# Optimization experiments

Hardware: AMD Instinct MI355X
Metric: run time of the kernel (lower is better)

Reference implementation:

```python
import jax, jax.numpy as jnp
import numpy as np

EPS = 1e-6  # flax LayerNorm default

def _layernorm(x, scale, bias):
    mu = jnp.mean(x, axis=-1, keepdims=True)
    var = jnp.mean(jnp.square(x - mu), axis=-1, keepdims=True)
    return (x - mu) * jax.lax.rsqrt(var + EPS) * scale + bias

def _rel_pos_index(ws):
    coords = np.stack(np.meshgrid(np.arange(ws), np.arange(ws), indexing='ij'))  # [2,ws,ws]
    cf = coords.reshape(2, -1)
    rel = (cf[:, :, None] - cf[:, None, :]).transpose(1, 2, 0)  # [N,N,2]
    rel[..., 0] += ws - 1
    rel[..., 1] += ws - 1
    rel[..., 0] *= 2 * ws - 1
    return rel.sum(-1)  # [N,N] in [0,(2ws-1)^2)

def setup_inputs() -> dict:
    key = jax.random.key(0)
    ks = jax.random.split(key, 8)
    B, H, W, C = 16, 56, 56, 384
    L, heads, ws = 2, 12, 7
    s = 0.02
    return {
        'x': jax.random.normal(ks[0], (B, H, W, C), jnp.float32),
        'ln1_s': jnp.ones((L, C), jnp.float32),
        'ln1_b': jnp.zeros((L, C), jnp.float32),
        'qkv_w': jax.random.normal(ks[1], (L, C, 3 * C), jnp.float32) * s,
        'rpb': jax.random.normal(ks[2], (L, (2 * ws - 1) ** 2, heads), jnp.float32) * s,
        'proj_w': jax.random.normal(ks[3], (L, C, C), jnp.float32) * s,
        'ln2_s': jnp.ones((L, C), jnp.float32),
        'ln2_b': jnp.zeros((L, C), jnp.float32),
        'mlp_w1': jax.random.normal(ks[4], (L, C, 4 * C), jnp.float32) * s,
        'mlp_b1': jnp.zeros((L, 4 * C), jnp.float32),
        'mlp_w2': jax.random.normal(ks[5], (L, 4 * C, C), jnp.float32) * s,
        'mlp_b2': jnp.zeros((L, C), jnp.float32),
        'window_size': 7,
    }

def reference(x, ln1_s, ln1_b, qkv_w, rpb, proj_w, ln2_s, ln2_b, mlp_w1, mlp_b1, mlp_w2, mlp_b2, window_size):
    B, H, W, C = x.shape
    ws = int(window_size)
    L = qkv_w.shape[0]
    heads = rpb.shape[-1]
    hd = C // heads
    N = ws * ws
    idx = jnp.asarray(_rel_pos_index(ws))  # [N,N] static

    # --- split to windows: [B,H,W,C] -> [B*nWh*nWw, N, C]
    xw = x.reshape(B, H // ws, ws, W // ws, ws, C)
    xw = xw.transpose(0, 1, 3, 2, 4, 5).reshape(-1, N, C)

    for l in range(L):
        # --- windowed MHSA with relative position bias
        h = _layernorm(xw, ln1_s[l], ln1_b[l])
        qkv = (h @ qkv_w[l]).reshape(-1, N, 3, heads, hd)
        q, k, v = qkv[:, :, 0], qkv[:, :, 1], qkv[:, :, 2]  # [nW,N,heads,hd]
        attn = jnp.einsum('wqhd,wkhd->whqk', q, k) * (hd ** -0.5)
        bias = rpb[l][idx].transpose(2, 0, 1)  # [heads,N,N]
        attn = jax.nn.softmax(attn + bias[None], axis=-1)
        o = jnp.einsum('whqk,wkhd->wqhd', attn, v).reshape(-1, N, C)
        xw = xw + o @ proj_w[l]
        # --- MLP block
        h = _layernorm(xw, ln2_s[l], ln2_b[l])
        h = jax.nn.gelu(h @ mlp_w1[l] + mlp_b1[l])
        xw = xw + (h @ mlp_w2[l] + mlp_b2[l])

    # --- merge windows back to [B,H,W,C]
    out = xw.reshape(B, H // ws, W // ws, ws, ws, C)
    out = out.transpose(0, 1, 3, 2, 4, 5).reshape(B, H, W, C)
    return out
```

## Files before the change

kernel.cpp:

```cpp
#include <hip/hip_runtime.h>
#include <hip/hip_bf16.h>

typedef __bf16 bf16;
typedef __attribute__((ext_vector_type(4))) __bf16 bf16x4;
typedef __attribute__((ext_vector_type(8))) __bf16 bf16x8;
typedef __attribute__((ext_vector_type(4))) float f32x4;

__device__ __forceinline__ void async_ld16(const void* g, void* l) {
    __builtin_amdgcn_global_load_lds(
        (const __attribute__((address_space(1))) unsigned int*)g,
        (__attribute__((address_space(3))) unsigned int*)l, 16, 0, 0);
}

__global__ __launch_bounds__(256) void k_f2bt(const float* __restrict__ in,
                                              bf16* __restrict__ out, int Kd, int Nd) {
    size_t loff = (size_t)blockIdx.y * Kd * Nd;
    int id = blockIdx.x * 256 + threadIdx.x;
    if (id >= Kd * Nd) return;
    int k = id / Nd, n = id - k * Nd;
    out[loff + (size_t)n * Kd + k] = (bf16)in[loff + id];
}

__global__ __launch_bounds__(256) void k_aux(const float* __restrict__ rpb,
                                             unsigned short* __restrict__ ridx,
                                             float* __restrict__ rpbT) {
    int e = blockIdx.x * 256 + threadIdx.x;
    if (e < 2401) {
        int i = e / 49, j = e - i * 49;
        int yi = i / 7, xi = i - yi * 7, yj = j / 7, xj = j - yj * 7;
        ridx[e] = (unsigned short)((yi - yj + 6) * 13 + (xi - xj + 6));
    }
    if (e < 4056) {
        int l = e / 2028, r = e - l * 2028;
        int h = r / 169, p = r - h * 169;
        rpbT[e] = rpb[l * 2028 + p * 12 + h];
    }
}

__global__ __launch_bounds__(256) void k_lnr(const float* __restrict__ x,
                                             const float* __restrict__ s,
                                             const float* __restrict__ b,
                                             float* __restrict__ xres,
                                             bf16* __restrict__ h) {
    int traw = blockIdx.x * 4 + (threadIdx.x >> 6);
    int lane = threadIdx.x & 63;
    int bb = traw / 3136;
    int rem = traw - bb * 3136;
    int y = rem / 56, xc = rem - y * 56;
    int w = bb * 64 + (y / 7) * 8 + (xc / 7);
    int n = (y % 7) * 7 + (xc % 7);
    int twin = w * 49 + n;

    const float4* row = (const float4*)(x + (size_t)traw * 384);
    float4 v0 = row[lane];
    float4 v1 = make_float4(0.f, 0.f, 0.f, 0.f);
    if (lane < 32) v1 = row[64 + lane];
    float sum = v0.x + v0.y + v0.z + v0.w + v1.x + v1.y + v1.z + v1.w;
#pragma unroll
    for (int m = 1; m < 64; m <<= 1) sum += __shfl_xor(sum, m);
    float mu = sum * (1.f / 384.f);
    float sq = (v0.x - mu) * (v0.x - mu) + (v0.y - mu) * (v0.y - mu) +
               (v0.z - mu) * (v0.z - mu) + (v0.w - mu) * (v0.w - mu);
    if (lane < 32)
        sq += (v1.x - mu) * (v1.x - mu) + (v1.y - mu) * (v1.y - mu) +
              (v1.z - mu) * (v1.z - mu) + (v1.w - mu) * (v1.w - mu);
#pragma unroll
    for (int m = 1; m < 64; m <<= 1) sq += __shfl_xor(sq, m);
    float r = rsqrtf(sq * (1.f / 384.f) + 1e-6f);

    float4* xr = (float4*)(xres + (size_t)twin * 384);
    const float4* s4 = (const float4*)s;
    const float4* b4 = (const float4*)b;
    bf16* ho = h + (size_t)twin * 384;
    {
        xr[lane] = v0;
        float4 sv = s4[lane], bv = b4[lane];
        bf16x4 ov;
        ov[0] = (bf16)((v0.x - mu) * r * sv.x + bv.x);
        ov[1] = (bf16)((v0.y - mu) * r * sv.y + bv.y);
        ov[2] = (bf16)((v0.z - mu) * r * sv.z + bv.z);
        ov[3] = (bf16)((v0.w - mu) * r * sv.w + bv.w);
        *(bf16x4*)&ho[lane * 4] = ov;
    }
    if (lane < 32) {
        xr[64 + lane] = v1;
        float4 sv = s4[64 + lane], bv = b4[64 + lane];
        bf16x4 ov;
        ov[0] = (bf16)((v1.x - mu) * r * sv.x + bv.x);
        ov[1] = (bf16)((v1.y - mu) * r * sv.y + bv.y);
        ov[2] = (bf16)((v1.z - mu) * r * sv.z + bv.z);
        ov[3] = (bf16)((v1.w - mu) * r * sv.w + bv.w);
        *(bf16x4*)&ho[256 + lane * 4] = ov;
    }
}

__global__ __launch_bounds__(256) void k_ln(const float* __restrict__ xres,
                                            const float* __restrict__ s,
                                            const float* __restrict__ b,
                                            bf16* __restrict__ h) {
    int t = blockIdx.x * 4 + (threadIdx.x >> 6);
    int lane = threadIdx.x & 63;
    const float4* row = (const float4*)(xres + (size_t)t * 384);
    float4 v0 = row[lane];
    float4 v1 = make_float4(0.f, 0.f, 0.f, 0.f);
    if (lane < 32) v1 = row[64 + lane];
    float sum = v0.x + v0.y + v0.z + v0.w + v1.x + v1.y + v1.z + v1.w;
#pragma unroll
    for (int m = 1; m < 64; m <<= 1) sum += __shfl_xor(sum, m);
    float mu = sum * (1.f / 384.f);
    float sq = (v0.x - mu) * (v0.x - mu) + (v0.y - mu) * (v0.y - mu) +
               (v0.z - mu) * (v0.z - mu) + (v0.w - mu) * (v0.w - mu);
    if (lane < 32)
        sq += (v1.x - mu) * (v1.x - mu) + (v1.y - mu) * (v1.y - mu) +
              (v1.z - mu) * (v1.z - mu) + (v1.w - mu) * (v1.w - mu);
#pragma unroll
    for (int m = 1; m < 64; m <<= 1) sq += __shfl_xor(sq, m);
    float r = rsqrtf(sq * (1.f / 384.f) + 1e-6f);
    const float4* s4 = (const float4*)s;
    const float4* b4 = (const float4*)b;
    bf16* ho = h + (size_t)t * 384;
    {
        float4 sv = s4[lane], bv = b4[lane];
        bf16x4 ov;
        ov[0] = (bf16)((v0.x - mu) * r * sv.x + bv.x);
        ov[1] = (bf16)((v0.y - mu) * r * sv.y + bv.y);
        ov[2] = (bf16)((v0.z - mu) * r * sv.z + bv.z);
        ov[3] = (bf16)((v0.w - mu) * r * sv.w + bv.w);
        *(bf16x4*)&ho[lane * 4] = ov;
    }
    if (lane < 32) {
        float4 sv = s4[64 + lane], bv = b4[64 + lane];
        bf16x4 ov;
        ov[0] = (bf16)((v1.x - mu) * r * sv.x + bv.x);
        ov[1] = (bf16)((v1.y - mu) * r * sv.y + bv.y);
        ov[2] = (bf16)((v1.z - mu) * r * sv.z + bv.z);
        ov[3] = (bf16)((v1.w - mu) * r * sv.w + bv.w);
        *(bf16x4*)&ho[256 + lane * 4] = ov;
    }
}

__device__ inline float gelu_f(float x) {
    float u = 0.7978845608028654f * (x + 0.044715f * x * x * x);
    float t = 1.f - 2.f / (__expf(2.f * u) + 1.f);
    return 0.5f * x * (1.f + t);
}

template <int EPI>
__global__ __launch_bounds__(256) void k_gemm(const bf16* __restrict__ A,
                                              const bf16* __restrict__ Bt,
                                              const float* __restrict__ bias,
                                              float* __restrict__ resid,
                                              bf16* __restrict__ Cout,
                                              float* __restrict__ outf,
                                              int N, int K) {
    __shared__ __align__(16) char lds[49152];
    int tid = threadIdx.x;

    int nwg = gridDim.x * gridDim.y;
    int orig = blockIdx.y * gridDim.x + blockIdx.x;
    int q = nwg >> 3, r8 = nwg & 7;
    int xcd = orig & 7, idx = orig >> 3;
    int wg = (xcd < r8 ? xcd * (q + 1) : r8 * (q + 1) + (xcd - r8) * q) + idx;
    int n0 = (wg % gridDim.x) * 128;
    int m0 = (wg / gridDim.x) * 128;

    int wave = tid >> 6, lane = tid & 63;
    int wm = (wave >> 1) * 64, wn = (wave & 1) * 64;
    int col = lane & 15, quad = lane >> 4;

    f32x4 acc[4][4] = {};

    int r0 = 2 * wave * 16 + (lane >> 2);
    int ksl = (lane & 3) ^ ((r0 >> 1) & 3);
    const bf16* ga0 = A + (size_t)(m0 + r0) * K + ksl * 8;
    const bf16* gb0 = Bt + (size_t)(n0 + r0) * K + ksl * 8;
    size_t rowK16 = (size_t)16 * K;
    int ldsoff = 2 * wave * 512;

    int NT = K >> 5;

    auto stage = [&](int t, int b) {
        const bf16* a = ga0 + t * 32;
        const bf16* g = gb0 + t * 32;
        char* base = (char*)lds + b * 16384;
        bf16* Ab = (bf16*)base;
        bf16* Bb = (bf16*)(base + 8192);
        async_ld16(a, Ab + ldsoff);
        async_ld16(a + rowK16, Ab + ldsoff + 512);
        async_ld16(g, Bb + ldsoff);
        async_ld16(g + rowK16, Bb + ldsoff + 512);
    };

    stage(0, 0);
    stage(1, 1);

    int buf = 0;
    for (int t = 0; t < NT; ++t) {
        if (t < NT - 1)
            asm volatile("s_waitcnt vmcnt(4) lgkmcnt(0)\n\ts_barrier" ::: "memory");
        else
            asm volatile("s_waitcnt vmcnt(0) lgkmcnt(0)\n\ts_barrier" ::: "memory");

        if (t + 2 < NT) {
            int sb = buf + 2; if (sb >= 3) sb -= 3;
            stage(t + 2, sb);
        }

        const char* base = (const char*)lds + buf * 16384;
        const bf16* Ab = (const bf16*)base;
        const bf16* Bb = (const bf16*)(base + 8192);
        bf16x8 af[4], bfv[4];
#pragma unroll
        for (int i = 0; i < 4; i++) {
            int ra = wm + i * 16 + col;
            af[i] = *(const bf16x8*)&Ab[ra * 32 + ((quad ^ ((ra >> 1) & 3)) << 3)];
            int rb = wn + i * 16 + col;
            bfv[i] = *(const bf16x8*)&Bb[rb * 32 + ((quad ^ ((rb >> 1) & 3)) << 3)];
        }
#pragma unroll
        for (int mi = 0; mi < 4; mi++)
#pragma unroll
            for (int ni = 0; ni < 4; ni++)
                acc[mi][ni] = __builtin_amdgcn_mfma_f32_16x16x32_bf16(
                    af[mi], bfv[ni], acc[mi][ni], 0, 0, 0);
        buf = (buf == 2) ? 0 : buf + 1;
    }

    __syncthreads();
    float* scrw = (float*)lds + wave * (16 * 68);

    int prow = lane >> 3;
    int pc0 = (lane & 7) * 8;
#pragma unroll
    for (int mi = 0; mi < 4; mi++) {
#pragma unroll
        for (int ni = 0; ni < 4; ni++)
#pragma unroll
            for (int r = 0; r < 4; r++)
                scrw[(quad * 4 + r) * 68 + ni * 16 + col] = acc[mi][ni][r];
#pragma unroll
        for (int h = 0; h < 2; h++) {
            int lr = h * 8 + prow;
            const float* sp = scrw + lr * 68 + pc0;
            float4 u0 = *(const float4*)sp;
            float4 u1 = *(const float4*)(sp + 4);
            int gm = m0 + wm + mi * 16 + lr;
            int gn = n0 + wn + pc0;
            size_t off = (size_t)gm * N + gn;
            if (EPI == 0) {
                bf16x8 ov;
                ov[0] = (bf16)u0.x; ov[1] = (bf16)u0.y; ov[2] = (bf16)u0.z; ov[3] = (bf16)u0.w;
                ov[4] = (bf16)u1.x; ov[5] = (bf16)u1.y; ov[6] = (bf16)u1.z; ov[7] = (bf16)u1.w;
                *(bf16x8*)&Cout[off] = ov;
            } else if (EPI == 1) {
                float4 b0 = *(const float4*)&bias[gn];
                float4 b1 = *(const float4*)&bias[gn + 4];
                bf16x8 ov;
                ov[0] = (bf16)gelu_f(u0.x + b0.x); ov[1] = (bf16)gelu_f(u0.y + b0.y);
                ov[2] = (bf16)gelu_f(u0.z + b0.z); ov[3] = (bf16)gelu_f(u0.w + b0.w);
                ov[4] = (bf16)gelu_f(u1.x + b1.x); ov[5] = (bf16)gelu_f(u1.y + b1.y);
                ov[6] = (bf16)gelu_f(u1.z + b1.z); ov[7] = (bf16)gelu_f(u1.w + b1.w);
                *(bf16x8*)&Cout[off] = ov;
            } else if (EPI == 2) {
                float4 r0v = *(const float4*)&resid[off];
                float4 r1v = *(const float4*)&resid[off + 4];
                r0v.x += u0.x; r0v.y += u0.y; r0v.z += u0.z; r0v.w += u0.w;
                r1v.x += u1.x; r1v.y += u1.y; r1v.z += u1.z; r1v.w += u1.w;
                *(float4*)&resid[off] = r0v;
                *(float4*)&resid[off + 4] = r1v;
            } else if (EPI == 3) {
                float4 b0 = *(const float4*)&bias[gn];
                float4 b1 = *(const float4*)&bias[gn + 4];
                float4 r0v = *(const float4*)&resid[off];
                float4 r1v = *(const float4*)&resid[off + 4];
                r0v.x += u0.x + b0.x; r0v.y += u0.y + b0.y;
                r0v.z += u0.z + b0.z; r0v.w += u0.w + b0.w;
                r1v.x += u1.x + b1.x; r1v.y += u1.y + b1.y;
                r1v.z += u1.z + b1.z; r1v.w += u1.w + b1.w;
                *(float4*)&resid[off] = r0v;
                *(float4*)&resid[off + 4] = r1v;
            } else {
                float4 b0 = *(const float4*)&bias[gn];
                float4 b1 = *(const float4*)&bias[gn + 4];
                float4 r0v = *(const float4*)&resid[off];
                float4 r1v = *(const float4*)&resid[off + 4];
                r0v.x += u0.x + b0.x; r0v.y += u0.y + b0.y;
                r0v.z += u0.z + b0.z; r0v.w += u0.w + b0.w;
                r1v.x += u1.x + b1.x; r1v.y += u1.y + b1.y;
                r1v.z += u1.z + b1.z; r1v.w += u1.w + b1.w;
                int wdx = gm / 49, n = gm - wdx * 49;
                int bb = wdx >> 6, r64 = wdx & 63;
                int n7 = n / 7;
                int yy = (r64 >> 3) * 7 + n7;
                int xx = (r64 & 7) * 7 + (n - n7 * 7);
                size_t traw = ((size_t)((bb * 56 + yy) * 56 + xx)) * 384 + gn;
                *(float4*)&outf[traw] = r0v;
                *(float4*)&outf[traw + 4] = r1v;
            }
        }
    }
}

__global__ __launch_bounds__(256) void k_attn(const bf16* __restrict__ qkv,
                                              const unsigned short* __restrict__ ridx,
                                              const float* __restrict__ rpbT,
                                              bf16* __restrict__ o) {
    __shared__ unsigned short relIdx[2401];
    __shared__ float rpbs[4][169];
    __shared__ __align__(16) bf16 Vs[4][32 * 72];
    __shared__ __align__(16) bf16 Ps[4][64 * 72];

    int tid = threadIdx.x;
    int wave = tid >> 6, lane = tid & 63;
    int col = lane & 15, quad = lane >> 4;
    int w = blockIdx.x;
    int head = blockIdx.y * 4 + wave;
    const float scale = 0.17677669529663687f;

    for (int e = tid; e < 2401; e += 256) relIdx[e] = ridx[e];
    for (int e = lane; e < 169; e += 64) rpbs[wave][e] = rpbT[head * 169 + e];

    const bf16* base = qkv + (size_t)w * 49 * 1152 + head * 32;
    bf16* vsw = Vs[wave];
    bf16* psw = Ps[wave];

    bf16x4 z4 = {(bf16)0.f, (bf16)0.f, (bf16)0.f, (bf16)0.f};
    for (int e = lane; e < 576; e += 64) *(bf16x4*)&vsw[e * 4] = z4;
    for (int e = lane; e < 392; e += 64) {
        int j = e >> 3, d4 = (e & 7) * 4;
        bf16x4 vv = *(const bf16x4*)&base[768 + (size_t)j * 1152 + d4];
        vsw[(d4 + 0) * 72 + j] = vv[0];
        vsw[(d4 + 1) * 72 + j] = vv[1];
        vsw[(d4 + 2) * 72 + j] = vv[2];
        vsw[(d4 + 3) * 72 + j] = vv[3];
    }

    __syncthreads();

    bf16x8 qf[4], kf[4];
#pragma unroll
    for (int mi = 0; mi < 4; mi++) {
        size_t row = (size_t)(mi * 16 + col) * 1152 + quad * 8;
        qf[mi] = *(const bf16x8*)&base[row];
        kf[mi] = *(const bf16x8*)&base[384 + row];
    }

    f32x4 S[4][4] = {};
#pragma unroll
    for (int mi = 0; mi < 4; mi++)
#pragma unroll
        for (int nj = 0; nj < 4; nj++)
            S[mi][nj] = __builtin_amdgcn_mfma_f32_16x16x32_bf16(qf[mi], kf[nj], S[mi][nj], 0, 0, 0);

    float* rp = rpbs[wave];
#pragma unroll
    for (int mi = 0; mi < 4; mi++) {
#pragma unroll
        for (int r = 0; r < 4; r++) {
            int ii = mi * 16 + quad * 4 + r;
            int ir = (ii < 49 ? ii : 0) * 49;
            float sv[4];
            float mx = -1e30f;
#pragma unroll
            for (int nj = 0; nj < 4; nj++) {
                int j = nj * 16 + col;
                float v;
                if (j < 49) v = S[mi][nj][r] * scale + rp[relIdx[ir + j]];
                else v = -1e30f;
                sv[nj] = v;
                mx = fmaxf(mx, v);
            }
#pragma unroll
            for (int m = 1; m < 16; m <<= 1) mx = fmaxf(mx, __shfl_xor(mx, m));
            float sum = 0.f;
#pragma unroll
            for (int nj = 0; nj < 4; nj++) {
                float p = __expf(sv[nj] - mx);
                sv[nj] = p;
                sum += p;
            }
#pragma unroll
            for (int m = 1; m < 16; m <<= 1) sum += __shfl_xor(sum, m);
            float is = 1.f / sum;
#pragma unroll
            for (int nj = 0; nj < 4; nj++)
                psw[ii * 72 + nj * 16 + col] = (bf16)(sv[nj] * is);
        }
    }

    __syncthreads();

    f32x4 O[4][2] = {};
#pragma unroll
    for (int kt = 0; kt < 2; kt++) {
        bf16x8 vb[2];
#pragma unroll
        for (int nt = 0; nt < 2; nt++)
            vb[nt] = *(const bf16x8*)&vsw[(nt * 16 + col) * 72 + kt * 32 + quad * 8];
#pragma unroll
        for (int mi = 0; mi < 4; mi++) {
            bf16x8 pa = *(const bf16x8*)&psw[(mi * 16 + col) * 72 + kt * 32 + quad * 8];
#pragma unroll
            for (int nt = 0; nt < 2; nt++)
                O[mi][nt] = __builtin_amdgcn_mfma_f32_16x16x32_bf16(pa, vb[nt], O[mi][nt], 0, 0, 0);
        }
    }

    bf16* ob = o + (size_t)w * 49 * 384 + head * 32;
#pragma unroll
    for (int mi = 0; mi < 4; mi++) {
#pragma unroll
        for (int r = 0; r < 4; r++) {
            int i = mi * 16 + quad * 4 + r;
            if (i < 49) {
#pragma unroll
                for (int nt = 0; nt < 2; nt++)
                    ob[(size_t)i * 384 + nt * 16 + col] = (bf16)O[mi][nt][r];
            }
        }
    }
}

extern "C" void kernel_launch(void* const* d_in, const int* in_sizes, int n_in,
                              void* d_out, int out_size, void* d_ws, size_t ws_size,
                              hipStream_t stream) {
    const float* x      = (const float*)d_in[0];
    const float* ln1_s  = (const float*)d_in[1];
    const float* ln1_b  = (const float*)d_in[2];
    const float* qkv_w  = (const float*)d_in[3];
    const float* rpb    = (const float*)d_in[4];
    const float* proj_w = (const float*)d_in[5];
    const float* ln2_s  = (const float*)d_in[6];
    const float* ln2_b  = (const float*)d_in[7];
    const float* mlp_w1 = (const float*)d_in[8];
    const float* mlp_b1 = (const float*)d_in[9];
    const float* mlp_w2 = (const float*)d_in[10];
    const float* mlp_b2 = (const float*)d_in[11];
    float* out = (float*)d_out;

    char* ws = (char*)d_ws;
    float* xres  = (float*)ws;
    bf16* qkvbuf = (bf16*)(ws + 77070336);
    bf16* obuf   = (bf16*)(ws + 192675840);
    bf16* wbuf   = (bf16*)(ws + 231211008);
    bf16* hidden = qkvbuf;
    bf16* hbuf   = (bf16*)d_out;

    unsigned short* ridx = (unsigned short*)((char*)d_out + 40000000);
    float* rpbT          = (float*)((char*)d_out + 40016384);

    bf16* qkvw_b  = wbuf;
    bf16* projw_b = wbuf + 884736;
    bf16* mlp1_b  = wbuf + 1179648;
    bf16* mlp2_b  = wbuf + 2359296;

    k_f2bt<<<dim3(1728, 2), 256, 0, stream>>>(qkv_w, qkvw_b, 384, 1152);
    k_f2bt<<<dim3(576, 2), 256, 0, stream>>>(proj_w, projw_b, 384, 384);
    k_f2bt<<<dim3(2304, 2), 256, 0, stream>>>(mlp_w1, mlp1_b, 384, 1536);
    k_f2bt<<<dim3(2304, 2), 256, 0, stream>>>(mlp_w2, mlp2_b, 1536, 384);
    k_aux<<<16, 256, 0, stream>>>(rpb, ridx, rpbT);

    k_lnr<<<12544, 256, 0, stream>>>(x, ln1_s, ln1_b, xres, hbuf);

    for (int l = 0; l < 2; l++) {
        k_gemm<0><<<dim3(9, 392), 256, 0, stream>>>(
            hbuf, qkvw_b + (size_t)l * 442368, nullptr, nullptr, qkvbuf, nullptr, 1152, 384);
        k_attn<<<dim3(1024, 3), 256, 0, stream>>>(qkvbuf, ridx, rpbT + l * 2028, obuf);
        k_gemm<2><<<dim3(3, 392), 256, 0, stream>>>(
            obuf, projw_b + (size_t)l * 147456, nullptr, xres, nullptr, nullptr, 384, 384);
        k_ln<<<12544, 256, 0, stream>>>(xres, ln2_s + l * 384, ln2_b + l * 384, hbuf);
        k_gemm<1><<<dim3(12, 392), 256, 0, stream>>>(
            hbuf, mlp1_b + (size_t)l * 589824, mlp_b1 + l * 1536, nullptr, hidden, nullptr, 1536, 384);
        if (l == 0) {
            k_gemm<3><<<dim3(3, 392), 256, 0, stream>>>(
                hidden, mlp2_b, mlp_b2, xres, nullptr, nullptr, 384, 1536);
            k_ln<<<12544, 256, 0, stream>>>(xres, ln1_s + 384, ln1_b + 384, hbuf);
        } else {
            k_gemm<4><<<dim3(3, 392), 256, 0, stream>>>(
                hidden, mlp2_b + 589824, mlp_b2 + 384, xres, nullptr, out, 384, 1536);
        }
    }
}
```

Baseline: 1.061 ms.

## Add 256x128-tile GEMM with triple-buffered LDS for QKV and MLP1

Adds a new GEMM kernel with a 256x128 output tile per workgroup (each wave computing 128x64), a three-stage async global-to-LDS pipeline, and an XCD-aware remapping of workgroup ids. It is used for the QKV projection and the first MLP layer, which halves the grid along M. The aim is more reuse of each loaded tile and better L2 locality per XCD. The cost is higher register pressure from 128 accumulator vectors per lane and 72KB of LDS per block, which limits occupancy.

New measurement: 1.091 ms. 1.03x slower.

```diff
diff --git a/kernel.cpp b/kernel.cpp
--- a/kernel.cpp
+++ b/kernel.cpp
@@ -301,6 +301,133 @@
     }
 }
 
+template <int EPI>
+__global__ __launch_bounds__(256, 2) void k_gemm_w(const bf16* __restrict__ A,
+                                                   const bf16* __restrict__ Bt,
+                                                   const float* __restrict__ bias,
+                                                   float* __restrict__ resid,
+                                                   bf16* __restrict__ Cout,
+                                                   float* __restrict__ outf,
+                                                   int N, int K) {
+    __shared__ __align__(16) char lds[73728];
+    int tid = threadIdx.x;
+
+    int nwg = gridDim.x * gridDim.y;
+    int orig = blockIdx.y * gridDim.x + blockIdx.x;
+    int q = nwg >> 3, r8 = nwg & 7;
+    int xcd = orig & 7, idx = orig >> 3;
+    int wg = (xcd < r8 ? xcd * (q + 1) : r8 * (q + 1) + (xcd - r8) * q) + idx;
+    int n0 = (wg % gridDim.x) * 128;
+    int m0 = (wg / gridDim.x) * 256;
+
+    int wave = tid >> 6, lane = tid & 63;
+    int wm = (wave >> 1) * 128, wn = (wave & 1) * 64;
+    int col = lane & 15, quad = lane >> 4;
+
+    f32x4 acc[8][4] = {};
+
+    int rr = lane >> 2;
+    int ksl = (lane & 3) ^ ((rr >> 1) & 3);
+    const bf16* ga0 = A + (size_t)(m0 + 64 * wave + rr) * K + ksl * 8;
+    const bf16* gb0 = Bt + (size_t)(n0 + 32 * wave + rr) * K + ksl * 8;
+    size_t rowK16 = (size_t)16 * K;
+    int ldsA = wave * 2048;
+    int ldsB = wave * 1024;
+
+    int NT = K >> 5;
+
+    auto stage = [&](int t, int b) {
+        const bf16* a = ga0 + t * 32;
+        const bf16* g = gb0 + t * 32;
+        char* base = (char*)lds + b * 24576;
+        bf16* Ab = (bf16*)base;
+        bf16* Bb = (bf16*)(base + 16384);
+        async_ld16(a, Ab + ldsA);
+        async_ld16(a + rowK16, Ab + ldsA + 512);
+        async_ld16(a + 2 * rowK16, Ab + ldsA + 1024);
+        async_ld16(a + 3 * rowK16, Ab + ldsA + 1536);
+        async_ld16(g, Bb + ldsB);
+        async_ld16(g + rowK16, Bb + ldsB + 512);
+    };
+
+    stage(0, 0);
+    stage(1, 1);
+
+    int buf = 0;
+    for (int t = 0; t < NT; ++t) {
+        if (t < NT - 1)
+            asm volatile("s_waitcnt vmcnt(6) lgkmcnt(0)\n\ts_barrier" ::: "memory");
+        else
+            asm volatile("s_waitcnt vmcnt(0) lgkmcnt(0)\n\ts_barrier" ::: "memory");
+
+        if (t + 2 < NT) {
+            int sb = buf + 2; if (sb >= 3) sb -= 3;
+            stage(t + 2, sb);
+        }
+
+        const char* base = (const char*)lds + buf * 24576;
+        const bf16* Ab = (const bf16*)base;
+        const bf16* Bb = (const bf16*)(base + 16384);
+        bf16x8 af[8], bfv[4];
+#pragma unroll
+        for (int i = 0; i < 8; i++) {
+            int ra = wm + i * 16 + col;
+            af[i] = *(const bf16x8*)&Ab[ra * 32 + ((quad ^ ((ra >> 1) & 3)) << 3)];
+        }
+#pragma unroll
+        for (int i = 0; i < 4; i++) {
+            int rb = wn + i * 16 + col;
+            bfv[i] = *(const bf16x8*)&Bb[rb * 32 + ((quad ^ ((rb >> 1) & 3)) << 3)];
+        }
+#pragma unroll
+        for (int mi = 0; mi < 8; mi++)
+#pragma unroll
+            for (int ni = 0; ni < 4; ni++)
+                acc[mi][ni] = __builtin_amdgcn_mfma_f32_16x16x32_bf16(
+                    af[mi], bfv[ni], acc[mi][ni], 0, 0, 0);
+        buf = (buf == 2) ? 0 : buf + 1;
+    }
+
+    __syncthreads();
+    float* scrw = (float*)lds + wave * (16 * 68);
+
+    int prow = lane >> 3;
+    int pc0 = (lane & 7) * 8;
+#pragma unroll
+    for (int mi = 0; mi < 8; mi++) {
+#pragma unroll
+        for (int ni = 0; ni < 4; ni++)
+#pragma unroll
+            for (int r = 0; r < 4; r++)
+                scrw[(quad * 4 + r) * 68 + ni * 16 + col] = acc[mi][ni][r];
+#pragma unroll
+        for (int h = 0; h < 2; h++) {
+            int lr = h * 8 + prow;
+            const float* sp = scrw + lr * 68 + pc0;
+            float4 u0 = *(const float4*)sp;
+            float4 u1 = *(const float4*)(sp + 4);
+            int gm = m0 + wm + mi * 16 + lr;
+            int gn = n0 + wn + pc0;
+            size_t off = (size_t)gm * N + gn;
+            if (EPI == 0) {
+                bf16x8 ov;
+                ov[0] = (bf16)u0.x; ov[1] = (bf16)u0.y; ov[2] = (bf16)u0.z; ov[3] = (bf16)u0.w;
+                ov[4] = (bf16)u1.x; ov[5] = (bf16)u1.y; ov[6] = (bf16)u1.z; ov[7] = (bf16)u1.w;
+                *(bf16x8*)&Cout[off] = ov;
+            } else {
+                float4 b0 = *(const float4*)&bias[gn];
+                float4 b1 = *(const float4*)&bias[gn + 4];
+                bf16x8 ov;
+                ov[0] = (bf16)gelu_f(u0.x + b0.x); ov[1] = (bf16)gelu_f(u0.y + b0.y);
+                ov[2] = (bf16)gelu_f(u0.z + b0.z); ov[3] = (bf16)gelu_f(u0.w + b0.w);
+                ov[4] = (bf16)gelu_f(u1.x + b1.x); ov[5] = (bf16)gelu_f(u1.y + b1.y);
+                ov[6] = (bf16)gelu_f(u1.z + b1.z); ov[7] = (bf16)gelu_f(u1.w + b1.w);
+                *(bf16x8*)&Cout[off] = ov;
+            }
+        }
+    }
+}
+
 __global__ __launch_bounds__(256) void k_attn(const bf16* __restrict__ qkv,
                                               const unsigned short* __restrict__ ridx,
                                               const float* __restrict__ rpbT,
@@ -463,13 +590,13 @@
     k_lnr<<<12544, 256, 0, stream>>>(x, ln1_s, ln1_b, xres, hbuf);
 
     for (int l = 0; l < 2; l++) {
-        k_gemm<0><<<dim3(9, 392), 256, 0, stream>>>(
+        k_gemm_w<0><<<dim3(9, 196), 256, 0, stream>>>(
             hbuf, qkvw_b + (size_t)l * 442368, nullptr, nullptr, qkvbuf, nullptr, 1152, 384);
         k_attn<<<dim3(1024, 3), 256, 0, stream>>>(qkvbuf, ridx, rpbT + l * 2028, obuf);
         k_gemm<2><<<dim3(3, 392), 256, 0, stream>>>(
             obuf, projw_b + (size_t)l * 147456, nullptr, xres, nullptr, nullptr, 384, 384);
         k_ln<<<12544, 256, 0, stream>>>(xres, ln2_s + l * 384, ln2_b + l * 384, hbuf);
-        k_gemm<1><<<dim3(12, 392), 256, 0, stream>>>(
+        k_gemm_w<1><<<dim3(12, 196), 256, 0, stream>>>(
             hbuf, mlp1_b + (size_t)l * 589824, mlp_b1 + l * 1536, nullptr, hidden, nullptr, 1536, 384);
         if (l == 0) {
             k_gemm<3><<<dim3(3, 392), 256, 0, stream>>>(
```

## Load GEMM B operand directly into registers and halve LDS footprint

Applied to the files above, without the earlier changes.

The GEMM no longer stages the weight (B) tile through LDS. Each wave now loads its B fragments straight from global memory into registers and prefetches the next k-step one iteration ahead. Only A stays triple-buffered in LDS, so shared memory drops to 24KB and launch bounds now request 4 blocks per CU, aiming for higher occupancy and less LDS traffic. In exchange, waves sharing the same columns fetch B redundantly from cache, and the extra in-flight register loads raise register pressure and vmcnt bookkeeping.

Measured after the change: 1.348 ms. +27.1%, slower.

```diff
diff --git a/kernel.cpp b/kernel.cpp
--- a/kernel.cpp
+++ b/kernel.cpp
@@ -146,14 +146,14 @@
 }
 
 template <int EPI>
-__global__ __launch_bounds__(256) void k_gemm(const bf16* __restrict__ A,
-                                              const bf16* __restrict__ Bt,
-                                              const float* __restrict__ bias,
-                                              float* __restrict__ resid,
-                                              bf16* __restrict__ Cout,
-                                              float* __restrict__ outf,
-                                              int N, int K) {
-    __shared__ __align__(16) char lds[49152];
+__global__ __launch_bounds__(256, 4) void k_gemm(const bf16* __restrict__ A,
+                                                 const bf16* __restrict__ Bt,
+                                                 const float* __restrict__ bias,
+                                                 float* __restrict__ resid,
+                                                 bf16* __restrict__ Cout,
+                                                 float* __restrict__ outf,
+                                                 int N, int K) {
+    __shared__ __align__(16) char lds[24576];
     int tid = threadIdx.x;
 
     int nwg = gridDim.x * gridDim.y;
@@ -173,61 +173,65 @@
     int r0 = 2 * wave * 16 + (lane >> 2);
     int ksl = (lane & 3) ^ ((r0 >> 1) & 3);
     const bf16* ga0 = A + (size_t)(m0 + r0) * K + ksl * 8;
-    const bf16* gb0 = Bt + (size_t)(n0 + r0) * K + ksl * 8;
     size_t rowK16 = (size_t)16 * K;
     int ldsoff = 2 * wave * 512;
 
+    const bf16* gB = Bt + (size_t)(n0 + wn + col) * K + quad * 8;
+    size_t fr16 = (size_t)16 * K;
+
     int NT = K >> 5;
 
-    auto stage = [&](int t, int b) {
+    auto stageA = [&](int t, int b) {
         const bf16* a = ga0 + t * 32;
-        const bf16* g = gb0 + t * 32;
-        char* base = (char*)lds + b * 16384;
-        bf16* Ab = (bf16*)base;
-        bf16* Bb = (bf16*)(base + 8192);
+        bf16* Ab = (bf16*)(lds + b * 8192);
         async_ld16(a, Ab + ldsoff);
         async_ld16(a + rowK16, Ab + ldsoff + 512);
-        async_ld16(g, Bb + ldsoff);
-        async_ld16(g + rowK16, Bb + ldsoff + 512);
     };
 
-    stage(0, 0);
-    stage(1, 1);
+    stageA(0, 0);
+    stageA(1, 1);
+    bf16x8 bcur[4], bnxt[4];
+#pragma unroll
+    for (int i = 0; i < 4; i++) bcur[i] = *(const bf16x8*)(gB + i * fr16);
 
     int buf = 0;
     for (int t = 0; t < NT; ++t) {
         if (t < NT - 1)
+            asm volatile("s_waitcnt vmcnt(6) lgkmcnt(0)\n\ts_barrier" ::: "memory");
+        else
             asm volatile("s_waitcnt vmcnt(4) lgkmcnt(0)\n\ts_barrier" ::: "memory");
-        else
-            asm volatile("s_waitcnt vmcnt(0) lgkmcnt(0)\n\ts_barrier" ::: "memory");
 
         if (t + 2 < NT) {
             int sb = buf + 2; if (sb >= 3) sb -= 3;
-            stage(t + 2, sb);
-        }
-
-        const char* base = (const char*)lds + buf * 16384;
-        const bf16* Ab = (const bf16*)base;
-        const bf16* Bb = (const bf16*)(base + 8192);
-        bf16x8 af[4], bfv[4];
+            stageA(t + 2, sb);
+        }
+        if (t + 1 < NT) {
+            const bf16* gb = gB + (t + 1) * 32;
+#pragma unroll
+            for (int i = 0; i < 4; i++) bnxt[i] = *(const bf16x8*)(gb + i * fr16);
+        }
+
+        const bf16* Ab = (const bf16*)(lds + buf * 8192);
+        bf16x8 af[4];
 #pragma unroll
         for (int i = 0; i < 4; i++) {
             int ra = wm + i * 16 + col;
             af[i] = *(const bf16x8*)&Ab[ra * 32 + ((quad ^ ((ra >> 1) & 3)) << 3)];
-            int rb = wn + i * 16 + col;
-            bfv[i] = *(const bf16x8*)&Bb[rb * 32 + ((quad ^ ((rb >> 1) & 3)) << 3)];
         }
 #pragma unroll
         for (int mi = 0; mi < 4; mi++)
 #pragma unroll
             for (int ni = 0; ni < 4; ni++)
                 acc[mi][ni] = __builtin_amdgcn_mfma_f32_16x16x32_bf16(
-                    af[mi], bfv[ni], acc[mi][ni], 0, 0, 0);
+                    af[mi], bcur[ni], acc[mi][ni], 0, 0, 0);
+#pragma unroll
+        for (int i = 0; i < 4; i++) bcur[i] = bnxt[i];
         buf = (buf == 2) ? 0 : buf + 1;
     }
 
     __syncthreads();
-    float* scrw = (float*)lds + wave * (16 * 68);
+    float* scrw = (float*)lds + wave * (16 * 68) / 4 * 4;
+    scrw = (float*)lds + wave * (16 * 68);
 
     int prow = lane >> 3;
     int pc0 = (lane & 7) * 8;
```
